# Kernel tuning notes

Hardware: AMD Instinct MI355X
Metric: run time of the kernel (lower is better)

Reference implementation:

```python
import jax, jax.numpy as jnp
import numpy as np

B, S, T = 8, 128, 4096
NX, NY = 256, 256
DX, DY = 1e-3, 1e-3
VS = 1550.0
DT = 1e-7


def setup_inputs() -> dict:
    key = jax.random.key(0)
    k1, k2 = jax.random.split(key)
    sensor_data = jax.random.normal(k1, (B, S, T), dtype=jnp.float32)
    sensor_xy = jax.random.randint(k2, (S, 2), 0, 256, dtype=jnp.int32)  # (S, 2) grid coords
    return {"sensor_data": sensor_data, "sensor_xy": sensor_xy}


def reference(sensor_data, sensor_xy):
    # sensor_data: (B, S, T) float32; sensor_xy: (S, 2) int grid positions
    b, s, t_len = sensor_data.shape
    ix = jnp.arange(NX, dtype=jnp.float32)  # zero-based pixel rows (== torch's x-idx+1)
    iy = jnp.arange(NY, dtype=jnp.float32)  # zero-based pixel cols
    x = sensor_xy[:, 0].astype(jnp.float32)[:, None, None]  # (S,1,1)
    y = sensor_xy[:, 1].astype(jnp.float32)[:, None, None]
    # Euclidean distance from each sensor to each pixel: (S, NX, NY)
    dis = jnp.sqrt(((x - ix[None, :, None]) * DX) ** 2 + ((y - iy[None, None, :]) * DY) ** 2)
    # time-of-flight index (truncation == floor, dis >= 0): (S, NX*NY)
    t = (dis / VS / DT).astype(jnp.int32).reshape(s, NX * NY)
    # gather-accumulate: image[b,p] = sum_s sensor_data[b, s, t[s,p]]
    idx = jnp.broadcast_to(t[None, :, :], (b, s, NX * NY))
    gathered = jnp.take_along_axis(sensor_data, idx, axis=2)  # (B, S, P)
    image = gathered.sum(axis=1)  # (B, P)
    # per-batch min-max normalization
    mn = image.min(axis=1, keepdims=True)
    mx = image.max(axis=1, keepdims=True)
    image = (image - mn) / (mx - mn)
    return image.reshape(b, NX, NY)
```

## Files before the change

### kernel.cpp

```cpp
#include <hip/hip_runtime.h>
#include <math.h>

constexpr int B = 8, S = 128, T = 4096;
constexpr int NPIX = 256 * 256;
constexpr float RVS = 1.0f / 1550.0f;
constexpr float RDT = 1.0e7f;
constexpr int NCHUNK = 8;
constexpr int SCHUNK = S / NCHUNK;
constexpr int WROWS = 160;
constexpr size_t PART_BYTES = (size_t)NPIX * B * sizeof(float);
constexpr size_t MM_OFF     = NCHUNK * PART_BYTES;
constexpr size_t WS_NEED    = MM_OFF + 256;

__device__ __forceinline__ int tof_index(int dxi, int dyi) {
    float ax = (float)dxi * 1e-3f;
    float ay = (float)dyi * 1e-3f;
    float px = ax * ax;
    float py = ay * ay;
    asm volatile("" : "+v"(px));
    asm volatile("" : "+v"(py));
    float d2  = px + py;
    float dis = __fsqrt_rn(d2);
    float q1  = __fmul_rn(dis, RVS);
    asm volatile("" : "+v"(q1));
    float tf  = __fmul_rn(q1, RDT);
    return (int)tf;
}

__device__ __forceinline__ unsigned fkey(float f) {
    unsigned u = __float_as_uint(f);
    return ((int)u < 0) ? ~u : (u | 0x80000000u);
}
__device__ __forceinline__ float funkey(unsigned k) {
    return __uint_as_float(((int)k < 0) ? (k ^ 0x80000000u) : ~k);
}


__global__ __launch_bounds__(256, 4) void das_accumw(const float* __restrict__ data,
                                                     const int* __restrict__ sxy,
                                                     float* __restrict__ part,
                                                     unsigned* __restrict__ mm) {
    __shared__ float win[B * WROWS];
    unsigned bid = blockIdx.x;
    int tid = threadIdx.x;
    if (bid == 0 && tid < 16) mm[tid] = (tid < 8) ? 0xFFFFFFFFu : 0u;

    int chunk = bid & 7;
    int tile  = bid >> 3;
    int tx0 = ((tile >> 4) << 4), ty0 = ((tile & 15) << 4);
    int l = tid & 63, w = tid >> 6;
    int ix = tx0 + ((w >> 1) << 3) + (l >> 3);
    int iy = ty0 + ((w & 1) << 3) + (l & 7);
    int p  = (ix << 8) + iy;

    float acc[B];
#pragma unroll
    for (int b = 0; b < B; ++b) acc[b] = 0.0f;

    int s0 = chunk * SCHUNK;
    for (int k = 0; k < SCHUNK; ++k) {
        int s = s0 + k;
        int x = sxy[2 * s], y = sxy[2 * s + 1];
        int dxi_min = max(0, max(tx0 - x, x - (tx0 + 15)));
        int dyi_min = max(0, max(ty0 - y, y - (ty0 + 15)));
        int tbase = tof_index(dxi_min, dyi_min) & ~3;

        __syncthreads();
        const float* srow = data + (size_t)s * T + tbase;
#pragma unroll
        for (int r = 0; r < 2; ++r) {
            int o4 = tid + r * 256;
            if (o4 < (B * WROWS) / 4) {
                int b  = o4 / (WROWS / 4);
                int t4 = o4 - b * (WROWS / 4);
                float4 v = *(const float4*)(srow + (size_t)b * (S * T) + t4 * 4);
                *(float4*)(&win[b * WROWS + t4 * 4]) = v;
            }
        }
        __syncthreads();

        int t = tof_index(abs(x - ix), abs(y - iy)) - tbase;
#pragma unroll
        for (int b = 0; b < B; ++b)
            acc[b] += win[b * WROWS + t];
    }

    float* dst = part + (size_t)chunk * NPIX * B;
#pragma unroll
    for (int b = 0; b < B; ++b)
        __builtin_nontemporal_store(acc[b], dst + b * NPIX + p);
}

__global__ __launch_bounds__(256) void das_combine(const float* __restrict__ part,
                                                   float* __restrict__ out,
                                                   unsigned* __restrict__ mm) {
    size_t i4 = ((size_t)blockIdx.x * 256 + threadIdx.x) * 4;
    int b = (int)(i4 >> 16);
    float4 v = make_float4(0.f, 0.f, 0.f, 0.f);
#pragma unroll
    for (int c = 0; c < NCHUNK; ++c) {
        const float* q = part + (size_t)c * NPIX * B + i4;
        v.x += __builtin_nontemporal_load(q);
        v.y += __builtin_nontemporal_load(q + 1);
        v.z += __builtin_nontemporal_load(q + 2);
        v.w += __builtin_nontemporal_load(q + 3);
    }
    *(float4*)(out + i4) = v;

    float mn = fminf(fminf(v.x, v.y), fminf(v.z, v.w));
    float mx = fmaxf(fmaxf(v.x, v.y), fmaxf(v.z, v.w));
    for (int off = 32; off; off >>= 1) {
        mn = fminf(mn, __shfl_down(mn, off));
        mx = fmaxf(mx, __shfl_down(mx, off));
    }
    __shared__ float smn[4], smx[4];
    int w = threadIdx.x >> 6;
    if ((threadIdx.x & 63) == 0) { smn[w] = mn; smx[w] = mx; }
    __syncthreads();
    if (threadIdx.x == 0) {
        mn = fminf(fminf(smn[0], smn[1]), fminf(smn[2], smn[3]));
        mx = fmaxf(fmaxf(smx[0], smx[1]), fmaxf(smx[2], smx[3]));
        atomicMin(&mm[b], fkey(mn));
        atomicMax(&mm[8 + b], fkey(mx));
    }
}

__global__ __launch_bounds__(256) void das_norm3(float* __restrict__ out,
                                                 const unsigned* __restrict__ mm) {
    size_t i4 = ((size_t)blockIdx.x * 256 + threadIdx.x) * 4;
    int b = (int)(i4 >> 16);
    float mn = funkey(mm[b]);
    float rs = __fsub_rn(funkey(mm[8 + b]), mn);
    float4 v = *(float4*)(out + i4);
    v.x = __fdiv_rn(__fsub_rn(v.x, mn), rs);
    v.y = __fdiv_rn(__fsub_rn(v.y, mn), rs);
    v.z = __fdiv_rn(__fsub_rn(v.z, mn), rs);
    v.w = __fdiv_rn(__fsub_rn(v.w, mn), rs);
    *(float4*)(out + i4) = v;
}


__global__ __launch_bounds__(256) void build_tab(unsigned short* __restrict__ tab) {
    int i = blockIdx.x * 256 + threadIdx.x;
    tab[i] = (unsigned short)tof_index(i >> 8, i & 255);
}

__global__ __launch_bounds__(256) void das_accum(const float* __restrict__ data,
                                                 const int* __restrict__ sxy,
                                                 const unsigned short* __restrict__ tab,
                                                 float* __restrict__ out) {
    __shared__ int sx[S], sy[S];
    int tid = threadIdx.x;
    if (tid < S) { sx[tid] = sxy[2 * tid]; sy[tid] = sxy[2 * tid + 1]; }
    __syncthreads();
    int b = blockIdx.x >> 8, ix = blockIdx.x & 255, iy = tid;
    int p = (ix << 8) + iy;
    const float* dbase = data + b * (S * T);
    double acc = 0.0;
#pragma unroll 8
    for (int s = 0; s < S; ++s) {
        int t = (int)tab[(abs(sx[s] - ix) << 8) + abs(sy[s] - iy)];
        acc += (double)dbase[s * T + t];
    }
    out[b * NPIX + p] = (float)acc;
}

__global__ __launch_bounds__(1024) void das_minmax(const float* __restrict__ img,
                                                   float* __restrict__ mmf) {
    int b = blockIdx.x;
    const float* p = img + b * NPIX;
    float mn = 3.0e38f, mx = -3.0e38f;
    for (int i = threadIdx.x; i < NPIX; i += 1024) {
        float v = p[i];
        mn = fminf(mn, v); mx = fmaxf(mx, v);
    }
    for (int off = 32; off; off >>= 1) {
        mn = fminf(mn, __shfl_down(mn, off));
        mx = fmaxf(mx, __shfl_down(mx, off));
    }
    __shared__ float smn[16], smx[16];
    int w = threadIdx.x >> 6;
    if ((threadIdx.x & 63) == 0) { smn[w] = mn; smx[w] = mx; }
    __syncthreads();
    if (threadIdx.x < 16) {
        mn = smn[threadIdx.x]; mx = smx[threadIdx.x];
        for (int off = 8; off; off >>= 1) {
            mn = fminf(mn, __shfl_down(mn, off));
            mx = fmaxf(mx, __shfl_down(mx, off));
        }
        if (threadIdx.x == 0) { mmf[2 * b] = mn; mmf[2 * b + 1] = mx; }
    }
}

__global__ __launch_bounds__(256) void das_norm(float* __restrict__ out,
                                                const float* __restrict__ mmf) {
    int i = blockIdx.x * 256 + threadIdx.x;
    int b = i >> 16;
    out[i] = __fdiv_rn(__fsub_rn(out[i], mmf[2 * b]), __fsub_rn(mmf[2 * b + 1], mmf[2 * b]));
}

extern "C" void kernel_launch(void* const* d_in, const int* in_sizes, int n_in,
                              void* d_out, int out_size, void* d_ws, size_t ws_size,
                              hipStream_t stream) {
    const float* data = (const float*)d_in[0];
    const int*   sxy  = (const int*)d_in[1];
    float* out = (float*)d_out;

    if (ws_size >= WS_NEED) {
        float*    part = (float*)d_ws;
        unsigned* mm   = (unsigned*)((char*)d_ws + MM_OFF);
        das_accumw<<<NCHUNK * 256, 256, 0, stream>>>(data, sxy, part, mm);
        das_combine<<<(B * NPIX) / 1024, 256, 0, stream>>>(part, out, mm);
        das_norm3<<<(B * NPIX) / 1024, 256, 0, stream>>>(out, mm);
    } else {
        unsigned short* tab = (unsigned short*)d_ws;
        float* mmf = (float*)((char*)d_ws + NPIX * sizeof(unsigned short));
        build_tab<<<NPIX / 256, 256, 0, stream>>>(tab);
        das_accum<<<B * 256, 256, 0, stream>>>(data, sxy, tab, out);
        das_minmax<<<B, 1024, 0, stream>>>(out, mmf);
        das_norm<<<(B * NPIX) / 256, 256, 0, stream>>>(out, mmf);
    }
}
```

Before: 39.74 us.

## Stage four sensors per barrier pair and halve sensor chunks

The accumulate kernel now loads windows for four sensors into shared memory between each pair of barriers instead of one. This cuts synchronisation count and exposes more independent global loads per thread. The number of sensor chunks drops from 8 to 4, which halves the partial buffers the combine kernel has to read but also halves the grid size. Shared memory grows to 20 KB per block, which may lower occupancy, and the combine kernel still loops over NCHUNK so it stays consistent.

```diff
diff --git a/kernel.cpp b/kernel.cpp
--- a/kernel.cpp
+++ b/kernel.cpp
@@ -5,9 +5,10 @@
 constexpr int NPIX = 256 * 256;
 constexpr float RVS = 1.0f / 1550.0f;
 constexpr float RDT = 1.0e7f;
-constexpr int NCHUNK = 8;
+constexpr int NCHUNK = 4;
 constexpr int SCHUNK = S / NCHUNK;
-constexpr int WROWS = 160;
+constexpr int GROUP  = 4;
+constexpr int WROWS  = 160;
 constexpr size_t PART_BYTES = (size_t)NPIX * B * sizeof(float);
 constexpr size_t MM_OFF     = NCHUNK * PART_BYTES;
 constexpr size_t WS_NEED    = MM_OFF + 256;
@@ -40,13 +41,13 @@
                                                      const int* __restrict__ sxy,
                                                      float* __restrict__ part,
                                                      unsigned* __restrict__ mm) {
-    __shared__ float win[B * WROWS];
+    __shared__ float win[GROUP * B * WROWS];
     unsigned bid = blockIdx.x;
     int tid = threadIdx.x;
     if (bid == 0 && tid < 16) mm[tid] = (tid < 8) ? 0xFFFFFFFFu : 0u;
 
-    int chunk = bid & 7;
-    int tile  = bid >> 3;
+    int chunk = bid & 3;
+    int tile  = bid >> 2;
     int tx0 = ((tile >> 4) << 4), ty0 = ((tile & 15) << 4);
     int l = tid & 63, w = tid >> 6;
     int ix = tx0 + ((w >> 1) << 3) + (l >> 3);
@@ -58,31 +59,44 @@
     for (int b = 0; b < B; ++b) acc[b] = 0.0f;
 
     int s0 = chunk * SCHUNK;
-    for (int k = 0; k < SCHUNK; ++k) {
-        int s = s0 + k;
-        int x = sxy[2 * s], y = sxy[2 * s + 1];
-        int dxi_min = max(0, max(tx0 - x, x - (tx0 + 15)));
-        int dyi_min = max(0, max(ty0 - y, y - (ty0 + 15)));
-        int tbase = tof_index(dxi_min, dyi_min) & ~3;
+    for (int k = 0; k < SCHUNK; k += GROUP) {
+        int xg[GROUP], yg[GROUP], tb[GROUP];
 
         __syncthreads();
-        const float* srow = data + (size_t)s * T + tbase;
-#pragma unroll
-        for (int r = 0; r < 2; ++r) {
-            int o4 = tid + r * 256;
-            if (o4 < (B * WROWS) / 4) {
-                int b  = o4 / (WROWS / 4);
-                int t4 = o4 - b * (WROWS / 4);
-                float4 v = *(const float4*)(srow + (size_t)b * (S * T) + t4 * 4);
-                *(float4*)(&win[b * WROWS + t4 * 4]) = v;
+#pragma unroll
+        for (int g = 0; g < GROUP; ++g) {
+            int s = s0 + k + g;
+            int x = sxy[2 * s], y = sxy[2 * s + 1];
+            int dxi_min = max(0, max(tx0 - x, x - (tx0 + 15)));
+            int dyi_min = max(0, max(ty0 - y, y - (ty0 + 15)));
+            int tbase = tof_index(dxi_min, dyi_min) & ~3;
+            xg[g] = x; yg[g] = y; tb[g] = tbase;
+
+            const float* srow = data + (size_t)s * T + tbase;
+            {
+                int o4 = tid;
+                int b  = o4 / 40;
+                int t4 = o4 - b * 40;
+                *(float4*)(&win[((g * B + b) * WROWS) + t4 * 4]) =
+                    *(const float4*)(srow + (size_t)b * (S * T) + t4 * 4);
+                o4 = tid + 256;
+                if (o4 < (B * WROWS) / 4) {
+                    b  = o4 / 40;
+                    t4 = o4 - b * 40;
+                    *(float4*)(&win[((g * B + b) * WROWS) + t4 * 4]) =
+                        *(const float4*)(srow + (size_t)b * (S * T) + t4 * 4);
+                }
             }
         }
         __syncthreads();
 
-        int t = tof_index(abs(x - ix), abs(y - iy)) - tbase;
-#pragma unroll
-        for (int b = 0; b < B; ++b)
-            acc[b] += win[b * WROWS + t];
+#pragma unroll
+        for (int g = 0; g < GROUP; ++g) {
+            int t = tof_index(abs(xg[g] - ix), abs(yg[g] - iy)) - tb[g];
+#pragma unroll
+            for (int b = 0; b < B; ++b)
+                acc[b] += win[(g * B + b) * WROWS + t];
+        }
     }
 
     float* dst = part + (size_t)chunk * NPIX * B;
```

After: 41.94 us. 1.06x slower.

## Double-buffer sensor windows in LDS, staging four sensors per barrier

Applied to the files above, without the earlier changes.

The accumulation kernel now loads the shared-memory time windows for four sensors at once into one of two ping-pong LDS buffers. It gathers from the other buffer while the next group loads, so each block uses 4 barriers instead of 32 and global loads overlap with LDS gathers. The cost is about 40KB of LDS per block, which may cap occupancy under the four-blocks-per-CU launch bound, plus higher register pressure from the unrolled macros.

```diff
diff --git a/kernel.cpp b/kernel.cpp
--- a/kernel.cpp
+++ b/kernel.cpp
@@ -7,7 +7,8 @@
 constexpr float RDT = 1.0e7f;
 constexpr int NCHUNK = 8;
 constexpr int SCHUNK = S / NCHUNK;
-constexpr int WROWS = 160;
+constexpr int GROUP  = 4;
+constexpr int WROWS  = 160;
 constexpr size_t PART_BYTES = (size_t)NPIX * B * sizeof(float);
 constexpr size_t MM_OFF     = NCHUNK * PART_BYTES;
 constexpr size_t WS_NEED    = MM_OFF + 256;
@@ -36,11 +37,49 @@
 }
 
 
+#define STAGE(KB, BUF) do {                                                  \
+    _Pragma("unroll")                                                        \
+    for (int g = 0; g < GROUP; ++g) {                                        \
+        int s = s0 + (KB) + g;                                               \
+        int x = sxy[2 * s], y = sxy[2 * s + 1];                              \
+        int dxm = max(0, max(tx0 - x, x - (tx0 + 15)));                      \
+        int dym = max(0, max(ty0 - y, y - (ty0 + 15)));                      \
+        int tbase = tof_index(dxm, dym) & ~3;                                \
+        const float* srow = data + (size_t)s * T + tbase;                    \
+        int o4 = tid;                                                        \
+        int bb = o4 / 40, t4 = o4 - bb * 40;                                 \
+        *(float4*)&BUF[(g * B + bb) * WROWS + t4 * 4] =                      \
+            *(const float4*)(srow + (size_t)bb * (S * T) + t4 * 4);          \
+        o4 = tid + 256;                                                      \
+        if (o4 < (B * WROWS) / 4) {                                          \
+            bb = o4 / 40; t4 = o4 - bb * 40;                                 \
+            *(float4*)&BUF[(g * B + bb) * WROWS + t4 * 4] =                  \
+                *(const float4*)(srow + (size_t)bb * (S * T) + t4 * 4);      \
+        }                                                                    \
+    }                                                                        \
+} while (0)
+
+#define GATHER(KB, BUF) do {                                                 \
+    _Pragma("unroll")                                                        \
+    for (int g = 0; g < GROUP; ++g) {                                        \
+        int s = s0 + (KB) + g;                                               \
+        int x = sxy[2 * s], y = sxy[2 * s + 1];                              \
+        int dxm = max(0, max(tx0 - x, x - (tx0 + 15)));                      \
+        int dym = max(0, max(ty0 - y, y - (ty0 + 15)));                      \
+        int tbase = tof_index(dxm, dym) & ~3;                                \
+        int t = tof_index(abs(x - ix), abs(y - iy)) - tbase;                 \
+        _Pragma("unroll")                                                    \
+        for (int bb = 0; bb < B; ++bb)                                       \
+            acc[bb] += BUF[(g * B + bb) * WROWS + t];                        \
+    }                                                                        \
+} while (0)
+
 __global__ __launch_bounds__(256, 4) void das_accumw(const float* __restrict__ data,
                                                      const int* __restrict__ sxy,
                                                      float* __restrict__ part,
                                                      unsigned* __restrict__ mm) {
-    __shared__ float win[B * WROWS];
+    __shared__ float win0[GROUP * B * WROWS];
+    __shared__ float win1[GROUP * B * WROWS];
     unsigned bid = blockIdx.x;
     int tid = threadIdx.x;
     if (bid == 0 && tid < 16) mm[tid] = (tid < 8) ? 0xFFFFFFFFu : 0u;
@@ -58,32 +97,16 @@
     for (int b = 0; b < B; ++b) acc[b] = 0.0f;
 
     int s0 = chunk * SCHUNK;
-    for (int k = 0; k < SCHUNK; ++k) {
-        int s = s0 + k;
-        int x = sxy[2 * s], y = sxy[2 * s + 1];
-        int dxi_min = max(0, max(tx0 - x, x - (tx0 + 15)));
-        int dyi_min = max(0, max(ty0 - y, y - (ty0 + 15)));
-        int tbase = tof_index(dxi_min, dyi_min) & ~3;
-
-        __syncthreads();
-        const float* srow = data + (size_t)s * T + tbase;
-#pragma unroll
-        for (int r = 0; r < 2; ++r) {
-            int o4 = tid + r * 256;
-            if (o4 < (B * WROWS) / 4) {
-                int b  = o4 / (WROWS / 4);
-                int t4 = o4 - b * (WROWS / 4);
-                float4 v = *(const float4*)(srow + (size_t)b * (S * T) + t4 * 4);
-                *(float4*)(&win[b * WROWS + t4 * 4]) = v;
-            }
-        }
-        __syncthreads();
-
-        int t = tof_index(abs(x - ix), abs(y - iy)) - tbase;
-#pragma unroll
-        for (int b = 0; b < B; ++b)
-            acc[b] += win[b * WROWS + t];
-    }
+
+    STAGE(0, win0);
+    __syncthreads();
+    STAGE(4, win1);  GATHER(0, win0);
+    __syncthreads();
+    STAGE(8, win0);  GATHER(4, win1);
+    __syncthreads();
+    STAGE(12, win1); GATHER(8, win0);
+    __syncthreads();
+    GATHER(12, win1);
 
     float* dst = part + (size_t)chunk * NPIX * B;
 #pragma unroll
```

Result: slower. 45.31 us (+14.0%).
